# Performance work log

Hardware: AMD Instinct MI355X
Metric: run time of the kernel (lower is better)

The kernel has to match this reference:

```python
import jax, jax.numpy as jnp
import numpy as np

D_MODEL = 512
D_INNER = 1024  # expand * d_model
D_STATE = 128
D_CONV = 4
DT_RANK = 32
DT_MIN, DT_MAX, DT_FLOOR = 0.001, 0.1, 1e-4


def setup_inputs() -> dict:
    key = jax.random.key(0)
    ks = jax.random.split(key, 8)
    B, S = 2, 1024
    return {
        "x": jax.random.normal(ks[0], (B, S, D_MODEL), jnp.float32),
        "W_in": jax.random.normal(ks[1], (D_MODEL, 2 * D_INNER), jnp.float32) * 0.02,
        "conv_w": jax.random.normal(ks[2], (D_INNER, 1, D_CONV), jnp.float32) * 0.1,
        "conv_b": jnp.zeros((D_INNER,), jnp.float32),
        "W_x": jax.random.normal(ks[3], (D_INNER, DT_RANK + 2 * D_STATE), jnp.float32) * 0.02,
        "W_dt": jax.random.normal(ks[4], (DT_RANK, D_INNER), jnp.float32) * 0.02,
        "b_dt": jnp.zeros((D_INNER,), jnp.float32),
        "W_out": jax.random.normal(ks[5], (D_INNER, D_MODEL), jnp.float32) * 0.02,
    }


def _mamba_forward(x, W_in, conv_w, conv_b, W_x, W_dt, b_dt, W_out):
    Bsz, S, _ = x.shape
    xr = x @ W_in                              # [B,S,2*d_inner]
    xs, res = jnp.split(xr, 2, axis=-1)        # each [B,S,d_inner]

    # depthwise causal conv (torch pads both sides by d_conv-1 then truncates
    # to seq_len, which equals a left-pad-only causal conv)
    xc = xs.transpose(0, 2, 1)                 # [B,d_inner,S]
    xc = jax.lax.conv_general_dilated(
        xc, conv_w, window_strides=(1,), padding=[(D_CONV - 1, 0)],
        feature_group_count=D_INNER)
    u = (xc + conv_b[None, :, None]).transpose(0, 2, 1)  # [B,S,d_inner]

    dbl = u @ W_x                              # [B,S,dt_rank+2*d_state]
    dt, Bm, Cm = jnp.split(dbl, [DT_RANK, DT_RANK + D_STATE], axis=-1)
    dt = dt @ W_dt + b_dt                      # [B,S,d_inner]
    dt = jnp.clip(jax.nn.softplus(dt + DT_FLOOR), DT_MIN, DT_MAX)

    # selective scan: h_t = h_{t-1}*(1-dt_t) + x_t (outer) B_t ; y_t = h_t . C_t
    def step(h, inp):
        x_t, dt_t, B_t, C_t = inp              # [B,d_inner],[B,d_inner],[B,N],[B,N]
        h = h * (1.0 - dt_t)[..., None] + x_t[..., None] * B_t[:, None, :]
        y = jnp.einsum('bdn,bn->bd', h, C_t)
        return h, y

    h0 = jnp.zeros((Bsz, D_INNER, D_STATE), u.dtype)
    xs_t = (u.transpose(1, 0, 2), dt.transpose(1, 0, 2),
            Bm.transpose(1, 0, 2), Cm.transpose(1, 0, 2))
    _, ys = jax.lax.scan(step, h0, xs_t)       # ys: [S,B,d_inner]

    y = ys.transpose(1, 0, 2) + res
    return y @ W_out                           # [B,S,d_model]


def reference(x, W_in, conv_w, conv_b, W_x, W_dt, b_dt, W_out):
    return _mamba_forward(x, W_in, conv_w, conv_b, W_x, W_dt, b_dt, W_out)
```

## Files before the change

kernel.cpp:

```cpp
#include <hip/hip_runtime.h>
#include <math.h>

#define S_LEN 1024
#define BATCH 2
#define DM 512
#define DI 1024
#define DS 128
#define DTR 32
#define CL 64
#define NC (S_LEN / CL)

typedef unsigned short ushortT;
typedef __attribute__((ext_vector_type(8))) short short8;
typedef __attribute__((ext_vector_type(4))) float f32x4;

__device__ __forceinline__ ushortT f2b(float f) {
  unsigned u = __builtin_bit_cast(unsigned, f);
  unsigned r = (u + 0x7fff + ((u >> 16) & 1)) >> 16;
  return (ushortT)r;
}
__device__ __forceinline__ float b2f(ushortT h) {
  return __builtin_bit_cast(float, (unsigned)h << 16);
}

#define GLOAD16(g, l)                                                     \
  __builtin_amdgcn_global_load_lds(                                       \
      (const __attribute__((address_space(1))) void*)(g),                 \
      (__attribute__((address_space(3))) void*)(l), 16, 0, 0)

template<int MODE>
__global__ __launch_bounds__(256) void gemm64(
    const ushortT* __restrict__ A, const ushortT* __restrict__ Bt,
    void* __restrict__ Cout, int N, int K, int ldc, int nbx) {
  __shared__ ushortT As[2][64 * 32];
  __shared__ ushortT Bs[2][64 * 32];
  const int nwg = gridDim.x;
  const int bid = blockIdx.x;
  const int flat = (bid & 7) * (nwg >> 3) + (bid >> 3);
  const int bxi = flat % nbx, byi = flat / nbx;
  const int bm = byi * 64, bn = bxi * 64;
  const int tid = threadIdx.x;
  const int l = tid & 63, w = tid >> 6;
  const int wr = w >> 1, wc = w & 1;
  const int srow = tid >> 2, scol = (tid & 3) * 8;
  const ushortT* gA = A + (size_t)(bm + srow) * K + scol;
  const ushortT* gB = Bt + (size_t)(bn + srow) * K + scol;
  f32x4 acc[2][2] = {};
  const int nt = K >> 5;
  GLOAD16(gA, &As[0][(size_t)tid * 8]);
  GLOAD16(gB, &Bs[0][(size_t)tid * 8]);
  __syncthreads();
  int cur = 0;
  for (int t = 0; t < nt; ++t) {
    if (t + 1 < nt) {
      GLOAD16(gA + (t + 1) * 32, &As[cur ^ 1][(size_t)tid * 8]);
      GLOAD16(gB + (t + 1) * 32, &Bs[cur ^ 1][(size_t)tid * 8]);
    }
    short8 a[2], b[2];
#pragma unroll
    for (int m = 0; m < 2; ++m)
      a[m] = *(const short8*)&As[cur][(wr * 32 + m * 16 + (l & 15)) * 32 + (l >> 4) * 8];
#pragma unroll
    for (int n = 0; n < 2; ++n)
      b[n] = *(const short8*)&Bs[cur][(wc * 32 + n * 16 + (l & 15)) * 32 + (l >> 4) * 8];
#pragma unroll
    for (int m = 0; m < 2; ++m)
#pragma unroll
      for (int n = 0; n < 2; ++n)
        acc[m][n] = __builtin_amdgcn_mfma_f32_16x16x32_bf16(a[m], b[n], acc[m][n], 0, 0, 0);
    __syncthreads();
    cur ^= 1;
  }
#pragma unroll
  for (int m = 0; m < 2; ++m) {
    int grow = bm + wr * 32 + m * 16 + (l >> 4) * 4;
#pragma unroll
    for (int n = 0; n < 2; ++n) {
      int gcol = bn + wc * 32 + n * 16 + (l & 15);
      if (gcol >= N) continue;
#pragma unroll
      for (int i = 0; i < 4; ++i) {
        float v = acc[m][n][i];
        if (MODE == 1)
          ((ushortT*)Cout)[(size_t)(grow + i) * ldc + gcol] = f2b(v);
        else
          ((float*)Cout)[(size_t)(grow + i) * ldc + gcol] = v;
      }
    }
  }
}

__global__ __launch_bounds__(256) void prep_all(
    const float* __restrict__ W_in, const float* __restrict__ W_x,
    const float* __restrict__ W_out, const float* __restrict__ x,
    ushortT* __restrict__ Wt_in, ushortT* __restrict__ Wt_x,
    ushortT* __restrict__ Wt_out, ushortT* __restrict__ x_bf) {
  __shared__ float tb[32][33];
  int bid = blockIdx.x;
  int tx = threadIdx.x, ty = threadIdx.y;
  const float* in; ushortT* out; int K, N, bx, by;
  if (bid < 1024)      { in = W_in;  out = Wt_in;  K = 512;  N = 2048; bx = bid & 63; by = bid >> 6; }
  else if (bid < 1408) { int t2 = bid - 1024; in = W_x;   out = Wt_x;   K = 1024; N = 288;  bx = t2 % 12; by = t2 / 12; }
  else if (bid < 1920) { int t2 = bid - 1408; in = W_out; out = Wt_out; K = 1024; N = 512;  bx = t2 % 16; by = t2 / 16; }
  else {
    int i = (bid - 1920) * 256 + ty * 32 + tx;
    float4 v = ((const float4*)x)[i];
    ushort4 o; o.x = f2b(v.x); o.y = f2b(v.y); o.z = f2b(v.z); o.w = f2b(v.w);
    ((ushort4*)x_bf)[i] = o;
    return;
  }
  int n0 = bx * 32, k0 = by * 32;
  int flat = ty * 32 + tx;
  if (n0 < N) {
#pragma unroll
    for (int i = 0; i < 4; ++i)
      tb[ty + 8 * i][tx] = in[(size_t)(k0 + ty + 8 * i) * N + n0 + tx];
    __syncthreads();
#pragma unroll
    for (int j = 0; j < 2; ++j) {
      int idx = j * 256 + flat;
      int r = idx >> 4, c2 = idx & 15;
      ushort2 o;
      o.x = f2b(tb[2 * c2][r]);
      o.y = f2b(tb[2 * c2 + 1][r]);
      *(ushort2*)&out[(size_t)(n0 + r) * K + k0 + 2 * c2] = o;
    }
  } else {
    ushort2 z; z.x = 0; z.y = 0;
#pragma unroll
    for (int j = 0; j < 2; ++j) {
      int idx = j * 256 + flat;
      int r = idx >> 4, c2 = idx & 15;
      *(ushort2*)&out[(size_t)(n0 + r) * K + k0 + 2 * c2] = z;
    }
  }
}

__global__ __launch_bounds__(256) void conv_kernel(
    const ushortT* __restrict__ xr, const float* __restrict__ w,
    const float* __restrict__ b, ushortT* __restrict__ u) {
  int idx = blockIdx.x * blockDim.x + threadIdx.x;
  int g = idx & 255;
  int s = (idx >> 8) & (S_LEN - 1);
  int bb = idx >> 18;
  int d = g * 4;
  float4 bias = *(const float4*)&b[d];
  float4 w0 = *(const float4*)&w[(d + 0) * 4];
  float4 w1 = *(const float4*)&w[(d + 1) * 4];
  float4 w2 = *(const float4*)&w[(d + 2) * 4];
  float4 w3 = *(const float4*)&w[(d + 3) * 4];
  float a0 = bias.x, a1 = bias.y, a2 = bias.z, a3 = bias.w;
  const ushortT* xs = xr + (size_t)(bb * S_LEN) * (2 * DI) + d;
#pragma unroll
  for (int k = 0; k < 4; ++k) {
    int si = s - 3 + k;
    if (si >= 0) {
      ushort4 v = *(const ushort4*)&xs[(size_t)si * (2 * DI)];
      float wk0 = ((const float*)&w0)[k], wk1 = ((const float*)&w1)[k];
      float wk2 = ((const float*)&w2)[k], wk3 = ((const float*)&w3)[k];
      a0 = fmaf(b2f(v.x), wk0, a0);
      a1 = fmaf(b2f(v.y), wk1, a1);
      a2 = fmaf(b2f(v.z), wk2, a2);
      a3 = fmaf(b2f(v.w), wk3, a3);
    }
  }
  ushort4 o; o.x = f2b(a0); o.y = f2b(a1); o.z = f2b(a2); o.w = f2b(a3);
  *(ushort4*)&u[(size_t)idx * 4] = o;
}

__global__ __launch_bounds__(256) void megachunk(
    const float* __restrict__ dbl, const float* __restrict__ W_dt,
    const float* __restrict__ b_dt, const ushortT* __restrict__ u_bf,
    ushortT* __restrict__ D, ushortT* __restrict__ ut,
    ushortT* __restrict__ zb) {
  __shared__ ushortT Btl[128][72];
  __shared__ float   Dl[64][66];
  __shared__ ushortT utl[64][72];
  __shared__ float   dtl[64][36];
  __shared__ ushortT Wl[32][68];
  const int t = threadIdx.x;
  const int dg = blockIdx.x, bc = blockIdx.y;
  const int b = bc >> 4, c = bc & 15;
  const size_t rowbase = (size_t)(b * S_LEN + c * CL) * DI + dg * 64;

#pragma unroll
  for (int j = 0; j < 8; ++j) {
    int idx4 = j * 256 + t;
    int s = idx4 >> 5, n4 = (idx4 & 31) * 4;
    float4 v = *(const float4*)&dbl[(size_t)(bc * 64 + s) * 288 + 32 + n4];
    Btl[n4][s] = f2b(v.x); Btl[n4 + 1][s] = f2b(v.y);
    Btl[n4 + 2][s] = f2b(v.z); Btl[n4 + 3][s] = f2b(v.w);
  }
#pragma unroll
  for (int j = 0; j < 2; ++j) {
    int idx4 = j * 256 + t;
    int s = idx4 >> 3, k4 = (idx4 & 7) * 4;
    *(float4*)&dtl[s][k4] = *(const float4*)&dbl[(size_t)(bc * 64 + s) * 288 + k4];
  }
#pragma unroll
  for (int j = 0; j < 4; ++j) {
    int idx2 = j * 256 + t;
    int k = idx2 >> 5, d2 = (idx2 & 31) * 2;
    float2 v = *(const float2*)&W_dt[(size_t)k * DI + dg * 64 + d2];
    Wl[k][d2] = f2b(v.x); Wl[k][d2 + 1] = f2b(v.y);
  }
  __syncthreads();

  {
    int d = t & 63, sq = t >> 6;
    float wreg[32];
#pragma unroll
    for (int k = 0; k < 32; ++k) wreg[k] = b2f(Wl[k][d]);
    float bias = b_dt[dg * 64 + d] + 1e-4f;
#pragma unroll 4
    for (int j = 0; j < 16; ++j) {
      int s = sq * 16 + j;
      float acc = bias;
#pragma unroll
      for (int k = 0; k < 32; ++k) acc = fmaf(dtl[s][k], wreg[k], acc);
      acc = (acc > 20.f) ? acc : log1pf(expf(acc));
      acc = fminf(fmaxf(acc, 0.001f), 0.1f);
      Dl[d][s] = 1.f - acc;
    }
  }
  __syncthreads();

  if (t < 64) {
    float cum = 1.f;
#pragma unroll 16
    for (int s = 0; s < CL; ++s) { cum *= Dl[t][s]; Dl[t][s] = cum; }
  }
  __syncthreads();

#pragma unroll
  for (int j = 0; j < 2; ++j) {
    int idx8 = j * 256 + t;
    int s = idx8 >> 3, d8 = (idx8 & 7) * 8;
    float4 raw = *(const float4*)&u_bf[rowbase + (size_t)s * DI + d8];
    const ushortT* up = (const ushortT*)&raw;
#pragma unroll
    for (int k = 0; k < 8; ++k)
      utl[d8 + k][s] = f2b(b2f(up[k]) / Dl[d8 + k][s]);
  }
  __syncthreads();

  {
    const int l = t & 63, w = t >> 6;
    f32x4 acc[8] = {};
#pragma unroll
    for (int kk = 0; kk < 2; ++kk) {
      short8 a = *(const short8*)&utl[w * 16 + (l & 15)][kk * 32 + (l >> 4) * 8];
#pragma unroll
      for (int n = 0; n < 8; ++n) {
        short8 bb = *(const short8*)&Btl[n * 16 + (l & 15)][kk * 32 + (l >> 4) * 8];
        acc[n] = __builtin_amdgcn_mfma_f32_16x16x32_bf16(a, bb, acc[n], 0, 0, 0);
      }
    }
#pragma unroll
    for (int n = 0; n < 8; ++n) {
      int gn = n * 16 + (l & 15);
#pragma unroll
      for (int i = 0; i < 4; ++i) {
        int d = dg * 64 + w * 16 + (l >> 4) * 4 + i;
        zb[(((size_t)(b * NC + c)) * DI + d) * 128 + gn] = f2b(acc[n][i]);
      }
    }
  }

#pragma unroll
  for (int j = 0; j < 2; ++j) {
    int idx8 = j * 256 + t;
    int s = idx8 >> 3, d8 = (idx8 & 7) * 8;
    float4 v; ushortT* vp = (ushortT*)&v;
#pragma unroll
    for (int k = 0; k < 8; ++k) vp[k] = f2b(Dl[d8 + k][s]);
    *(float4*)&D[rowbase + (size_t)s * DI + d8] = v;
  }
#pragma unroll
  for (int j = 0; j < 2; ++j) {
    int idx8 = j * 256 + t;
    int d = idx8 >> 3, s8 = (idx8 & 7) * 8;
    float4 v; ushortT* vp = (ushortT*)&v;
#pragma unroll
    for (int k = 0; k < 8; ++k) vp[k] = utl[d][s8 + k];
    *(float4*)&ut[((size_t)bc * DI + dg * 64 + d) * CL + s8] = v;
  }
}

__global__ __launch_bounds__(256) void scan_pass2(
    const ushortT* __restrict__ zb, const ushortT* __restrict__ D,
    ushortT* __restrict__ hstb) {
  int wid = (blockIdx.x * blockDim.x + threadIdx.x) >> 6;
  int lane = threadIdx.x & 63;
  int b = wid >> 10, d = wid & (DI - 1);
  float h0 = 0.f, h1 = 0.f;
#pragma unroll
  for (int c = 0; c < NC; ++c) {
    float dend = b2f(D[((size_t)(b * S_LEN + c * CL + CL - 1)) * DI + d]);
    size_t addr = (((size_t)(b * NC + c)) * DI + d) * 128 + 2 * lane;
    ushort2 z2 = *(const ushort2*)&zb[addr];
    ushort2 he;
    he.x = f2b(h0); he.y = f2b(h1);
    *(ushort2*)&hstb[addr] = he;
    h0 = dend * (h0 + b2f(z2.x));
    h1 = dend * (h1 + b2f(z2.y));
  }
}

__global__ __launch_bounds__(256) void gemm_y(
    const float* __restrict__ dbl, const ushortT* __restrict__ ut,
    const ushortT* __restrict__ hstb, const ushortT* __restrict__ D,
    const ushortT* __restrict__ xr_bf, ushortT* __restrict__ yr) {
  __shared__ ushortT Bl[64][136];
  __shared__ ushortT Cl[64][136];
  __shared__ ushortT Gl[64][72];
  __shared__ ushortT Ul[64][72];
  __shared__ ushortT Hl[64][136];
  __shared__ ushortT Dl2[64][72];
  const int tid = threadIdx.x;
  const int l = tid & 63, w = tid >> 6;
  const int bc = blockIdx.y, d0 = blockIdx.x * 64;
  const int b = bc >> 4, c = bc & 15;
  const int brow = b * S_LEN + c * CL;
#pragma unroll
  for (int j = 0; j < 2; ++j) {
    int idx4 = j * 256 + tid;
    int dr = idx4 >> 3, s8 = (idx4 & 7) * 8;
    float4 v = *(const float4*)&ut[((size_t)bc * DI + d0 + dr) * CL + s8];
    *(float4*)&Ul[dr][s8] = v;
  }
#pragma unroll
  for (int j = 0; j < 4; ++j) {
    int idx4 = j * 256 + tid;
    int dr = idx4 >> 4, n8 = (idx4 & 15) * 8;
    float4 v = *(const float4*)&hstb[(((size_t)(b * NC + c)) * DI + d0 + dr) * 128 + n8];
    *(float4*)&Hl[dr][n8] = v;
  }
#pragma unroll
  for (int j = 0; j < 2; ++j) {
    int idx4 = j * 256 + tid;
    int tr = idx4 >> 3, d8 = (idx4 & 7) * 8;
    float4 v = *(const float4*)&D[((size_t)(brow + tr)) * DI + d0 + d8];
    *(float4*)&Dl2[tr][d8] = v;
  }
#pragma unroll
  for (int j = 0; j < 16; ++j) {
    int idx4 = j * 256 + tid;
    int row = idx4 >> 6, c4 = (idx4 & 63) * 4;
    float4 v = *(const float4*)&dbl[(size_t)(bc * 64 + row) * 288 + 32 + c4];
    ushortT o0 = f2b(v.x), o1 = f2b(v.y), o2 = f2b(v.z), o3 = f2b(v.w);
    if (c4 < 128) { Bl[row][c4] = o0; Bl[row][c4+1] = o1; Bl[row][c4+2] = o2; Bl[row][c4+3] = o3; }
    else { int cc = c4 - 128; Cl[row][cc] = o0; Cl[row][cc+1] = o1; Cl[row][cc+2] = o2; Cl[row][cc+3] = o3; }
  }
  __syncthreads();
  {
    f32x4 gacc[4] = {};
#pragma unroll
    for (int kk = 0; kk < 4; ++kk) {
      short8 a = *(const short8*)&Cl[w * 16 + (l & 15)][kk * 32 + (l >> 4) * 8];
#pragma unroll
      for (int nf = 0; nf < 4; ++nf) {
        short8 bb = *(const short8*)&Bl[nf * 16 + (l & 15)][kk * 32 + (l >> 4) * 8];
        gacc[nf] = __builtin_amdgcn_mfma_f32_16x16x32_bf16(a, bb, gacc[nf], 0, 0, 0);
      }
    }
#pragma unroll
    for (int nf = 0; nf < 4; ++nf) {
      int s = nf * 16 + (l & 15);
#pragma unroll
      for (int i = 0; i < 4; ++i) {
        int tr = w * 16 + (l >> 4) * 4 + i;
        Gl[tr][s] = f2b((s <= tr) ? gacc[nf][i] : 0.f);
      }
    }
  }
  __syncthreads();
  f32x4 acc[4] = {};
#pragma unroll
  for (int kk = 0; kk < 2; ++kk) {
    short8 a = *(const short8*)&Gl[w * 16 + (l & 15)][kk * 32 + (l >> 4) * 8];
#pragma unroll
    for (int n = 0; n < 4; ++n) {
      short8 bb = *(const short8*)&Ul[n * 16 + (l & 15)][kk * 32 + (l >> 4) * 8];
      acc[n] = __builtin_amdgcn_mfma_f32_16x16x32_bf16(a, bb, acc[n], 0, 0, 0);
    }
  }
#pragma unroll
  for (int kk = 0; kk < 4; ++kk) {
    short8 a = *(const short8*)&Cl[w * 16 + (l & 15)][kk * 32 + (l >> 4) * 8];
#pragma unroll
    for (int n = 0; n < 4; ++n) {
      short8 bb = *(const short8*)&Hl[n * 16 + (l & 15)][kk * 32 + (l >> 4) * 8];
      acc[n] = __builtin_amdgcn_mfma_f32_16x16x32_bf16(a, bb, acc[n], 0, 0, 0);
    }
  }
#pragma unroll
  for (int n = 0; n < 4; ++n) {
    int dl = n * 16 + (l & 15);
    int d = d0 + dl;
#pragma unroll
    for (int i = 0; i < 4; ++i) {
      int tl = w * 16 + (l >> 4) * 4 + i;
      int gr = brow + tl;
      float Dv = b2f(Dl2[tl][dl]);
      float res = b2f(xr_bf[(size_t)gr * 2048 + 1024 + d]);
      yr[(size_t)gr * DI + d] = f2b(acc[n][i] * Dv + res);
    }
  }
}

extern "C" void kernel_launch(void* const* d_in, const int* in_sizes, int n_in,
                              void* d_out, int out_size, void* d_ws, size_t ws_size,
                              hipStream_t stream) {
  const float* x      = (const float*)d_in[0];
  const float* W_in   = (const float*)d_in[1];
  const float* conv_w = (const float*)d_in[2];
  const float* conv_b = (const float*)d_in[3];
  const float* W_x    = (const float*)d_in[4];
  const float* W_dt   = (const float*)d_in[5];
  const float* b_dt   = (const float*)d_in[6];
  const float* W_out  = (const float*)d_in[7];
  float* out = (float*)d_out;
  float* ws = (float*)d_ws;

  ushortT* xr_bf = (ushortT*)ws;
  ushortT* u_bf  = (ushortT*)(ws + 2097152);
  float*   dbl   = ws + 3145728;
  ushortT* Dc    = (ushortT*)(ws + 3735552);
  ushortT* ut    = (ushortT*)(ws + 5832704);
  ushortT* zb    = (ushortT*)(ws + 6881280);
  ushortT* hstb  = (ushortT*)(ws + 8978432);
  ushortT* x_bf  = (ushortT*)(ws + 11075584);
  ushortT* Wt_in = (ushortT*)(ws + 11599872);
  ushortT* Wt_x  = (ushortT*)(ws + 12124160);
  ushortT* Wt_out= (ushortT*)(ws + 12320768);
  ushortT* yr_bf = (ushortT*)(ws + 12582912);

  dim3 blk(256);
  prep_all<<<2944, dim3(32, 8), 0, stream>>>(W_in, W_x, W_out, x,
                                             Wt_in, Wt_x, Wt_out, x_bf);
  gemm64<1><<<1024, blk, 0, stream>>>(x_bf, Wt_in, xr_bf, 2 * DI, DM, 2 * DI, 32);
  conv_kernel<<<2048, blk, 0, stream>>>(xr_bf, conv_w, conv_b, u_bf);
  gemm64<0><<<160, blk, 0, stream>>>(u_bf, Wt_x, dbl, DTR + 2 * DS, DI, DTR + 2 * DS, 5);
  megachunk<<<dim3(16, 32), blk, 0, stream>>>(dbl, W_dt, b_dt, u_bf, Dc, ut, zb);
  scan_pass2<<<512, blk, 0, stream>>>(zb, Dc, hstb);
  gemm_y<<<dim3(16, 32), blk, 0, stream>>>(dbl, ut, hstb, Dc, xr_bf, yr_bf);
  gemm64<0><<<256, blk, 0, stream>>>(yr_bf, Wt_out, out, DM, DI, DM, 8);
}
```

Measured before the change: 94.13 us.

## Fuse chunk scan, inter-chunk pass and output GEMM into one cooperative kernel

Merges megachunk, scan_pass2 and gemm_y into a single cooperative kernel that uses grid-wide syncs between the phases. The D and ut tiles stay in shared memory instead of being written to and re-read from global memory, and only per-chunk decay totals (dend) are stored in fp32. The C·B^T Gram matrix is computed before the grid sync, and shared memory is overlaid across phases. This removes two launches and several global round trips, but adds two grid barriers and requires all 512 blocks to be co-resident.

```diff
diff --git a/kernel.cpp b/kernel.cpp
--- a/kernel.cpp
+++ b/kernel.cpp
@@ -1,5 +1,8 @@
 #include <hip/hip_runtime.h>
+#include <hip/hip_cooperative_groups.h>
 #include <math.h>
+
+namespace cg = cooperative_groups;
 
 #define S_LEN 1024
 #define BATCH 2
@@ -168,20 +171,30 @@
   *(ushort4*)&u[(size_t)idx * 4] = o;
 }
 
-__global__ __launch_bounds__(256) void megachunk(
+__global__ __launch_bounds__(256) void scan_fused(
     const float* __restrict__ dbl, const float* __restrict__ W_dt,
     const float* __restrict__ b_dt, const ushortT* __restrict__ u_bf,
-    ushortT* __restrict__ D, ushortT* __restrict__ ut,
-    ushortT* __restrict__ zb) {
-  __shared__ ushortT Btl[128][72];
+    float* __restrict__ dend, ushortT* __restrict__ zb,
+    ushortT* __restrict__ hstb, const ushortT* __restrict__ xr_bf,
+    ushortT* __restrict__ yr) {
   __shared__ float   Dl[64][66];
   __shared__ ushortT utl[64][72];
-  __shared__ float   dtl[64][36];
-  __shared__ ushortT Wl[32][68];
+  __shared__ __align__(16) char ovl[45056];
+  ushortT (*Btl)[72] = (ushortT(*)[72])ovl;
+  float   (*dtl)[36] = (float(*)[36])(ovl + 18432);
+  ushortT (*Wl)[68]  = (ushortT(*)[68])(ovl + 27648);
+  ushortT (*Cl)[136] = (ushortT(*)[136])ovl;
+  ushortT (*Bl)[136] = (ushortT(*)[136])(ovl + 17408);
+  ushortT (*Gl)[72]  = (ushortT(*)[72])(ovl + 34816);
+
   const int t = threadIdx.x;
-  const int dg = blockIdx.x, bc = blockIdx.y;
+  const int bid = blockIdx.x;
+  const int bc = bid & 31, dg = bid >> 5;
   const int b = bc >> 4, c = bc & 15;
+  const int l = t & 63, w = t >> 6;
   const size_t rowbase = (size_t)(b * S_LEN + c * CL) * DI + dg * 64;
+  const int brow = b * S_LEN + c * CL;
+  const int d0 = dg * 64;
 
 #pragma unroll
   for (int j = 0; j < 8; ++j) {
@@ -229,6 +242,7 @@
     float cum = 1.f;
 #pragma unroll 16
     for (int s = 0; s < CL; ++s) { cum *= Dl[t][s]; Dl[t][s] = cum; }
+    dend[((size_t)(b * DI) + dg * 64 + t) * 16 + c] = cum;
   }
   __syncthreads();
 
@@ -245,7 +259,6 @@
   __syncthreads();
 
   {
-    const int l = t & 63, w = t >> 6;
     f32x4 acc[8] = {};
 #pragma unroll
     for (int kk = 0; kk < 2; ++kk) {
@@ -266,86 +279,11 @@
       }
     }
   }
-
-#pragma unroll
-  for (int j = 0; j < 2; ++j) {
-    int idx8 = j * 256 + t;
-    int s = idx8 >> 3, d8 = (idx8 & 7) * 8;
-    float4 v; ushortT* vp = (ushortT*)&v;
-#pragma unroll
-    for (int k = 0; k < 8; ++k) vp[k] = f2b(Dl[d8 + k][s]);
-    *(float4*)&D[rowbase + (size_t)s * DI + d8] = v;
-  }
-#pragma unroll
-  for (int j = 0; j < 2; ++j) {
-    int idx8 = j * 256 + t;
-    int d = idx8 >> 3, s8 = (idx8 & 7) * 8;
-    float4 v; ushortT* vp = (ushortT*)&v;
-#pragma unroll
-    for (int k = 0; k < 8; ++k) vp[k] = utl[d][s8 + k];
-    *(float4*)&ut[((size_t)bc * DI + dg * 64 + d) * CL + s8] = v;
-  }
-}
-
-__global__ __launch_bounds__(256) void scan_pass2(
-    const ushortT* __restrict__ zb, const ushortT* __restrict__ D,
-    ushortT* __restrict__ hstb) {
-  int wid = (blockIdx.x * blockDim.x + threadIdx.x) >> 6;
-  int lane = threadIdx.x & 63;
-  int b = wid >> 10, d = wid & (DI - 1);
-  float h0 = 0.f, h1 = 0.f;
-#pragma unroll
-  for (int c = 0; c < NC; ++c) {
-    float dend = b2f(D[((size_t)(b * S_LEN + c * CL + CL - 1)) * DI + d]);
-    size_t addr = (((size_t)(b * NC + c)) * DI + d) * 128 + 2 * lane;
-    ushort2 z2 = *(const ushort2*)&zb[addr];
-    ushort2 he;
-    he.x = f2b(h0); he.y = f2b(h1);
-    *(ushort2*)&hstb[addr] = he;
-    h0 = dend * (h0 + b2f(z2.x));
-    h1 = dend * (h1 + b2f(z2.y));
-  }
-}
-
-__global__ __launch_bounds__(256) void gemm_y(
-    const float* __restrict__ dbl, const ushortT* __restrict__ ut,
-    const ushortT* __restrict__ hstb, const ushortT* __restrict__ D,
-    const ushortT* __restrict__ xr_bf, ushortT* __restrict__ yr) {
-  __shared__ ushortT Bl[64][136];
-  __shared__ ushortT Cl[64][136];
-  __shared__ ushortT Gl[64][72];
-  __shared__ ushortT Ul[64][72];
-  __shared__ ushortT Hl[64][136];
-  __shared__ ushortT Dl2[64][72];
-  const int tid = threadIdx.x;
-  const int l = tid & 63, w = tid >> 6;
-  const int bc = blockIdx.y, d0 = blockIdx.x * 64;
-  const int b = bc >> 4, c = bc & 15;
-  const int brow = b * S_LEN + c * CL;
-#pragma unroll
-  for (int j = 0; j < 2; ++j) {
-    int idx4 = j * 256 + tid;
-    int dr = idx4 >> 3, s8 = (idx4 & 7) * 8;
-    float4 v = *(const float4*)&ut[((size_t)bc * DI + d0 + dr) * CL + s8];
-    *(float4*)&Ul[dr][s8] = v;
-  }
-#pragma unroll
-  for (int j = 0; j < 4; ++j) {
-    int idx4 = j * 256 + tid;
-    int dr = idx4 >> 4, n8 = (idx4 & 15) * 8;
-    float4 v = *(const float4*)&hstb[(((size_t)(b * NC + c)) * DI + d0 + dr) * 128 + n8];
-    *(float4*)&Hl[dr][n8] = v;
-  }
-#pragma unroll
-  for (int j = 0; j < 2; ++j) {
-    int idx4 = j * 256 + tid;
-    int tr = idx4 >> 3, d8 = (idx4 & 7) * 8;
-    float4 v = *(const float4*)&D[((size_t)(brow + tr)) * DI + d0 + d8];
-    *(float4*)&Dl2[tr][d8] = v;
-  }
+  __syncthreads();
+
 #pragma unroll
   for (int j = 0; j < 16; ++j) {
-    int idx4 = j * 256 + tid;
+    int idx4 = j * 256 + t;
     int row = idx4 >> 6, c4 = (idx4 & 63) * 4;
     float4 v = *(const float4*)&dbl[(size_t)(bc * 64 + row) * 288 + 32 + c4];
     ushortT o0 = f2b(v.x), o1 = f2b(v.y), o2 = f2b(v.z), o3 = f2b(v.w);
@@ -374,6 +312,38 @@
       }
     }
   }
+
+  __threadfence();
+  cg::this_grid().sync();
+
+  {
+    int wid = bid * 4 + w;
+    int b2 = wid >> 10, d2 = wid & (DI - 1);
+    float h0 = 0.f, h1 = 0.f;
+#pragma unroll
+    for (int c2 = 0; c2 < NC; ++c2) {
+      float dd = dend[(size_t)wid * 16 + c2];
+      size_t addr = (((size_t)(b2 * NC + c2)) * DI + d2) * 128 + 2 * l;
+      ushort2 z2 = *(const ushort2*)&zb[addr];
+      ushort2 he;
+      he.x = f2b(h0); he.y = f2b(h1);
+      *(ushort2*)&hstb[addr] = he;
+      h0 = dd * (h0 + b2f(z2.x));
+      h1 = dd * (h1 + b2f(z2.y));
+    }
+  }
+
+  __threadfence();
+  cg::this_grid().sync();
+
+  ushortT (*Hl)[136] = Bl;
+#pragma unroll
+  for (int j = 0; j < 4; ++j) {
+    int idx4 = j * 256 + t;
+    int dr = idx4 >> 4, n8 = (idx4 & 15) * 8;
+    float4 v = *(const float4*)&hstb[(((size_t)(b * NC + c)) * DI + d0 + dr) * 128 + n8];
+    *(float4*)&Hl[dr][n8] = v;
+  }
   __syncthreads();
   f32x4 acc[4] = {};
 #pragma unroll
@@ -381,7 +351,7 @@
     short8 a = *(const short8*)&Gl[w * 16 + (l & 15)][kk * 32 + (l >> 4) * 8];
 #pragma unroll
     for (int n = 0; n < 4; ++n) {
-      short8 bb = *(const short8*)&Ul[n * 16 + (l & 15)][kk * 32 + (l >> 4) * 8];
+      short8 bb = *(const short8*)&utl[n * 16 + (l & 15)][kk * 32 + (l >> 4) * 8];
       acc[n] = __builtin_amdgcn_mfma_f32_16x16x32_bf16(a, bb, acc[n], 0, 0, 0);
     }
   }
@@ -402,7 +372,7 @@
     for (int i = 0; i < 4; ++i) {
       int tl = w * 16 + (l >> 4) * 4 + i;
       int gr = brow + tl;
-      float Dv = b2f(Dl2[tl][dl]);
+      float Dv = Dl[dl][tl];
       float res = b2f(xr_bf[(size_t)gr * 2048 + 1024 + d]);
       yr[(size_t)gr * DI + d] = f2b(acc[n][i] * Dv + res);
     }
@@ -426,8 +396,7 @@
   ushortT* xr_bf = (ushortT*)ws;
   ushortT* u_bf  = (ushortT*)(ws + 2097152);
   float*   dbl   = ws + 3145728;
-  ushortT* Dc    = (ushortT*)(ws + 3735552);
-  ushortT* ut    = (ushortT*)(ws + 5832704);
+  float*   dend  = ws + 3735552;
   ushortT* zb    = (ushortT*)(ws + 6881280);
   ushortT* hstb  = (ushortT*)(ws + 8978432);
   ushortT* x_bf  = (ushortT*)(ws + 11075584);
@@ -442,8 +411,12 @@
   gemm64<1><<<1024, blk, 0, stream>>>(x_bf, Wt_in, xr_bf, 2 * DI, DM, 2 * DI, 32);
   conv_kernel<<<2048, blk, 0, stream>>>(xr_bf, conv_w, conv_b, u_bf);
   gemm64<0><<<160, blk, 0, stream>>>(u_bf, Wt_x, dbl, DTR + 2 * DS, DI, DTR + 2 * DS, 5);
-  megachunk<<<dim3(16, 32), blk, 0, stream>>>(dbl, W_dt, b_dt, u_bf, Dc, ut, zb);
-  scan_pass2<<<512, blk, 0, stream>>>(zb, Dc, hstb);
-  gemm_y<<<dim3(16, 32), blk, 0, stream>>>(dbl, ut, hstb, Dc, xr_bf, yr_bf);
+  {
+    void* kargs[] = {(void*)&dbl, (void*)&W_dt, (void*)&b_dt, (void*)&u_bf,
+                     (void*)&dend, (void*)&zb, (void*)&hstb, (void*)&xr_bf,
+                     (void*)&yr_bf};
+    hipLaunchCooperativeKernel((const void*)scan_fused, dim3(512), dim3(256),
+                               kargs, 0, stream);
+  }
   gemm64<0><<<256, blk, 0, stream>>>(yr_bf, Wt_out, out, DM, DI, DM, 8);
 }
```

After: 267.2 us. +183.9%, slower.
